# Optimization experiments

Hardware: AMD Instinct MI355X
Metric: run time of the kernel (lower is better)

Reference implementation:

```python
import jax, jax.numpy as jnp
import numpy as np

NP = 4            # num_patches
P = NP * NP       # num_patches^2
BIG = 1e8         # self-distance sentinel used by the torch module
IN_CH = 128
MID = IN_CH // 2
NUM_CONVS = 3
KS = 3
B, H, W = 4, 256, 256


def conv2d(x, w, b):
    # x: [B,C,H,W], w: [O,I,kh,kw] (OIHW), stride 1, 'same' padding
    pad = (w.shape[-1] - 1) // 2
    y = jax.lax.conv_general_dilated(
        x, w, window_strides=(1, 1), padding=[(pad, pad), (pad, pad)],
        dimension_numbers=('NCHW', 'OIHW', 'NCHW'))
    return y + b[None, :, None, None]


def patchify(x):
    # [B,C,H,W] -> [B,P,C,hs,ws] with row-major patch order (i*NP+j)
    b, c, h, w = x.shape
    hs, ws = h // NP, w // NP
    x = x.reshape(b, c, NP, hs, NP, ws).transpose(0, 2, 4, 1, 3, 5)
    return x.reshape(b, P, c, hs, ws)


def unpatchify(xp, h, w):
    b, p, c, hs, ws = xp.shape
    x = xp.reshape(b, NP, NP, c, hs, ws).transpose(0, 3, 1, 4, 2, 5)
    return x.reshape(b, c, h, w)


def setup_inputs() -> dict:
    key = jax.random.key(0)
    ks = jax.random.split(key, 16)
    s = 0.05  # weight init scale (~kaiming for these fan-ins)
    inp = {
        'x':     jax.random.normal(ks[0], (B, IN_CH, H, W), jnp.float32),
        'pre_w': jax.random.normal(ks[1], (MID, IN_CH, KS, KS), jnp.float32) * s,
        'pre_b': jnp.zeros((MID,), jnp.float32),
        'c1_w':  jax.random.normal(ks[2], (NUM_CONVS, MID, MID, KS, KS), jnp.float32) * s,
        'c1_b':  jnp.zeros((NUM_CONVS, MID), jnp.float32),
        'c2_w':  jax.random.normal(ks[3], (NUM_CONVS, MID, MID, KS, KS), jnp.float32) * s,
        'c2_b':  jnp.zeros((NUM_CONVS, MID), jnp.float32),
        'p1_w':  jax.random.normal(ks[4], (P, MID, MID), jnp.float32) * s,  # [patch, out, in] 1x1 conv
        'p1_b':  jnp.zeros((P, MID), jnp.float32),
        'p2_w':  jax.random.normal(ks[5], (P, MID, MID), jnp.float32) * s,
        'p2_b':  jnp.zeros((P, MID), jnp.float32),
        'fin_w': jax.random.normal(ks[6], (IN_CH, IN_CH, KS, KS), jnp.float32) * s,
        'fin_b': jnp.zeros((IN_CH,), jnp.float32),
    }
    return inp


def reference(x, pre_w, pre_b, c1_w, c1_b, c2_w, c2_b,
              p1_w, p1_b, p2_w, p2_b, fin_w, fin_b):
    x0 = jax.nn.relu(conv2d(x, pre_w, pre_b))
    h1 = x0
    for i in range(c1_w.shape[0]):
        h1 = jax.nn.relu(conv2d(h1, c1_w[i], c1_b[i]))
    x1 = h1 + x0
    h2 = x0
    for i in range(c2_w.shape[0]):
        h2 = jax.nn.relu(conv2d(h2, c2_w[i], c2_b[i]))
    x2 = h2 + x0

    # per-patch 1x1 convs (all P patches batched via einsum)
    x1p = patchify(x1)  # [B,P,C,hs,ws]
    x2p = patchify(x2)
    x1p = jnp.einsum('bpchw,pdc->bpdhw', x1p, p1_w) + p1_b[None, :, :, None, None]
    x2p = jnp.einsum('bpchw,pdc->bpdhw', x2p, p2_w) + p2_b[None, :, :, None, None]

    # pairwise squared distances between x1 patches and x2 patches
    f1 = x1p.reshape(B, P, -1)
    f2 = x2p.reshape(B, P, -1)
    d = ((f1 ** 2).sum(-1)[:, :, None]
         + (f2 ** 2).sum(-1)[:, None, :]
         - 2.0 * jnp.einsum('bpd,bqd->bpq', f1, f2))  # [B,P,P]
    d = jnp.where(jnp.eye(P, dtype=bool)[None], BIG, d)
    # torch does softmax(exp(-d)) — keep the double transform faithfully
    attn = jax.nn.softmax(jnp.exp(-d), axis=-1)  # [B,P,P]

    outp = jnp.einsum('bpq,bqchw->bpchw', attn, x2p)
    out = unpatchify(outp, H, W)           # [B,MID,H,W]
    out = jnp.concatenate([out, x0], axis=1)  # [B,IN_CH,H,W]
    out = jax.nn.relu(conv2d(out, fin_w, fin_b))
    return out + x
```

## Files before the change

### kernel.cpp

```cpp
#include <hip/hip_runtime.h>
#include <hip/hip_bf16.h>

#define BB   4
#define HH   256
#define WW   256
#define INCH 128
#define MIDC 64
#define NPAT 4
#define PP   16
#define PS   64

typedef __bf16 bf16x8 __attribute__((ext_vector_type(8)));
typedef float f32x4 __attribute__((ext_vector_type(4)));
typedef unsigned short ushort_t;

#define UPL 16777216UL

__device__ inline ushort_t f2bf(float f) {
    unsigned u = __float_as_uint(f);
    unsigned r = (u + 0x7FFFu + ((u >> 16) & 1u)) >> 16;
    return (ushort_t)r;
}
__device__ inline float bf2f(ushort_t h) {
    return __uint_as_float(((unsigned)h) << 16);
}
__device__ inline f32x4 mfma16(uint4 a, uint4 b, f32x4 c) {
    return __builtin_amdgcn_mfma_f32_16x16x32_bf16(
        __builtin_bit_cast(bf16x8, a), __builtin_bit_cast(bf16x8, b), c, 0, 0, 0);
}

__global__ __launch_bounds__(256) void prep_all_kernel(
    const float* __restrict__ pre_w, const float* __restrict__ c1_w,
    const float* __restrict__ c2_w,  const float* __restrict__ fin_w,
    const float* __restrict__ p1_w,  const float* __restrict__ p2_w,
    const float* __restrict__ c1_b,  const float* __restrict__ c2_b,
    ushort_t* __restrict__ wpPre, ushort_t* __restrict__ wpC,
    ushort_t* __restrict__ wpFin, ushort_t* __restrict__ pw1b,
    ushort_t* __restrict__ pw2b,  float* __restrict__ zbuf,
    float* __restrict__ cbias)
{
    int idx = blockIdx.x * 256 + threadIdx.x;
    if (idx < 73728) {
        int tap = idx % 9, ci = (idx / 9) % 128, co = idx / 1152;
        wpPre[(tap * 64 + co) * 128 + ci] = f2bf(pre_w[idx]);
    } else if (idx < 294912) {
        int j = idx - 73728;
        int which = j / 36864, k = j % 36864;
        const float* src = (which < 3) ? (c1_w + (size_t)which * 36864)
                                       : (c2_w + (size_t)(which - 3) * 36864);
        int tap = k % 9, ci = (k / 9) % 64, co = k / 576;
        wpC[(size_t)which * 36864 + (tap * 64 + co) * 64 + ci] = f2bf(src[k]);
    } else if (idx < 442368) {
        int k = idx - 294912;
        int tap = k % 9, ci = (k / 9) % 128, co = k / 1152;
        wpFin[(tap * 128 + co) * 128 + ci] = f2bf(fin_w[k]);
    } else if (idx < 507904) {
        pw1b[idx - 442368] = f2bf(p1_w[idx - 442368]);
    } else if (idx < 573440) {
        pw2b[idx - 507904] = f2bf(p2_w[idx - 507904]);
    } else if (idx < 574592) {
        zbuf[idx - 573440] = 0.f;
    } else if (idx < 574784) {
        cbias[idx - 574592] = c1_b[idx - 574592];
    } else if (idx < 574976) {
        cbias[192 + idx - 574784] = c2_b[idx - 574784];
    }
}

__global__ __launch_bounds__(256) void x_to_nhwc_kernel(
    const float* __restrict__ x, ushort_t* __restrict__ xh)
{
    __shared__ ushort_t sm[64 * 136];
    const int t = threadIdx.x;
    const int bx = blockIdx.x;
    const int b = bx >> 10;
    const int pxbase = (bx & 1023) * 64;
#pragma unroll
    for (int i = 0; i < 32; ++i) {
        int idx = i * 256 + t;
        int c = idx >> 6, pxl = idx & 63;
        sm[pxl * 136 + c] = f2bf(x[((size_t)(b * 128 + c)) * 65536 + pxbase + pxl]);
    }
    __syncthreads();
#pragma unroll
    for (int i = 0; i < 4; ++i) {
        int idx = i * 256 + t;
        int pxl = idx >> 4, q = idx & 15;
        uint4 v = *(const uint4*)&sm[pxl * 136 + q * 8];
        *(uint4*)(xh + ((size_t)b * 65536 + pxbase + pxl) * 128 + q * 8) = v;
    }
}

template<int CIN, int CSPLIT>
__device__ inline void stage10x34(const ushort_t* inA, const ushort_t* inB,
                                  int b, int y0, int x0, int t, int cb,
                                  uint4 (&stg)[6])
{
#pragma unroll
    for (int i = 0; i < 6; ++i) {
        int e = i * 256 + t;
        int pxl = e >> 2, quad = e & 3;
        int row = pxl / 34, xl = pxl - row * 34;
        int gy = y0 + row - 1, gx = x0 + xl - 1;
        bool ok = (e < 1360) && ((unsigned)gy < 256u) && ((unsigned)gx < 256u);
        int c0 = cb + quad * 8;
        const ushort_t* src; int nch, ch;
        if ((CSPLIT == CIN) || (c0 < CSPLIT)) { src = inA; nch = CSPLIT; ch = c0; }
        else { src = inB; nch = CIN - CSPLIT; ch = c0 - CSPLIT; }
        uint4 v = make_uint4(0u, 0u, 0u, 0u);
        if (ok) v = *(const uint4*)(src + ((size_t)((b * 256 + gy) * 256 + gx)) * nch + ch);
        stg[i] = v;
    }
}

template<int CIN, int CSPLIT, int OMODE, bool PAIR, bool COPAIR>
__global__ __launch_bounds__(256) void mconv3x3(
    const ushort_t* __restrict__ inA, const ushort_t* __restrict__ inB,
    const ushort_t* __restrict__ wgtT,
    const float* __restrict__ bias,
    const void* __restrict__ res,
    void* __restrict__ out,
    int COUT, size_t inStride, size_t wStride, size_t bStride, size_t outStride)
{
    constexpr int NCH = CIN / 32;
    __shared__ ushort_t sm[10 * 34 * 36];

    const int t = threadIdx.x;
    const int nx = gridDim.x;
    const int bid = blockIdx.x;
    const int fid = (bid & 7) * (nx >> 3) + (bid >> 3);
    int tile, cog;
    if (COPAIR) { tile = fid >> 1; cog = (fid & 1) * 64; }
    else        { tile = fid;      cog = PAIR ? 0 : blockIdx.y * 64; }
    const int y0 = (tile >> 3) * 8;
    const int x0 = (tile & 7) * 32;
    const int br = PAIR ? blockIdx.y : 0;
    const ushort_t* inAb = inA + (size_t)br * inStride;
    const ushort_t* inBb = inB + (size_t)br * inStride;
    const ushort_t* wgt  = wgtT + (size_t)br * wStride;
    const float*    bs   = bias + (size_t)br * bStride;
    const int b = blockIdx.z;
    const int l = t & 63, w = t >> 6;
    const int lan15 = l & 15;
    const int g4 = l >> 4;
    const int k8 = g4 * 8;
    const int co0 = cog + (w & 1) * 32;
    const int xw = (w >> 1) * 16;

    f32x4 acc[2][8];
#pragma unroll
    for (int mt = 0; mt < 2; ++mt)
#pragma unroll
        for (int r = 0; r < 8; ++r) acc[mt][r] = (f32x4)0.f;

    uint4 stg[6];
    stage10x34<CIN, CSPLIT>(inAb, inBb, b, y0, x0, t, 0, stg);

    for (int cc = 0; cc < NCH; ++cc) {
        __syncthreads();
#pragma unroll
        for (int i = 0; i < 6; ++i) {
            int e = i * 256 + t;
            if (e < 1360) {
                int pxl = e >> 2, quad = e & 3;
                *(uint4*)&sm[pxl * 36 + quad * 8] = stg[i];
            }
        }
        __syncthreads();
        if (cc + 1 < NCH)
            stage10x34<CIN, CSPLIT>(inAb, inBb, b, y0, x0, t, (cc + 1) * 32, stg);

        const int cb = cc * 32;
        uint4 af[2][9];
#pragma unroll
        for (int mt = 0; mt < 2; ++mt)
#pragma unroll
            for (int tap = 0; tap < 9; ++tap)
                af[mt][tap] = *(const uint4*)(wgt +
                    ((size_t)tap * COUT + co0 + mt * 16 + lan15) * CIN + cb + k8);

#pragma unroll
        for (int s = 0; s < 10; ++s) {
#pragma unroll
            for (int dx = 0; dx < 3; ++dx) {
                const int pxl = s * 34 + xw + lan15 + dx;
                uint4 bv = *(const uint4*)&sm[pxl * 36 + k8];
#pragma unroll
                for (int dy = 0; dy < 3; ++dy) {
                    const int r = s - dy;
                    if (r >= 0 && r < 8) {
                        acc[0][r] = mfma16(af[0][dy * 3 + dx], bv, acc[0][r]);
                        acc[1][r] = mfma16(af[1][dy * 3 + dx], bv, acc[1][r]);
                    }
                }
            }
        }
    }

#pragma unroll
    for (int mt = 0; mt < 2; ++mt) {
#pragma unroll
        for (int r = 0; r < 8; ++r) {
            const int y = y0 + r;
            const int x = x0 + xw + lan15;
            const int codr = co0 + mt * 16 + g4 * 4;
            float v[4];
#pragma unroll
            for (int j = 0; j < 4; ++j)
                v[j] = fmaxf(acc[mt][r][j] + bs[codr + j], 0.f);
            if constexpr (OMODE == 2) {
                const float* rf = (const float*)res;
                float* of = (float*)out;
#pragma unroll
                for (int j = 0; j < 4; ++j) {
                    size_t oi = ((size_t)(b * COUT + codr + j) * 256 + y) * 256 + x;
                    of[oi] = v[j] + rf[oi];
                }
            } else {
                const size_t pix = (size_t)(b * 256 + y) * 256 + x;
                if constexpr (OMODE == 1) {
                    const ushort_t* rp = (const ushort_t*)res + pix * 64 + codr;
#pragma unroll
                    for (int j = 0; j < 4; ++j) v[j] += bf2f(rp[j]);
                }
                uint2 pk;
                pk.x = (unsigned)f2bf(v[0]) | ((unsigned)f2bf(v[1]) << 16);
                pk.y = (unsigned)f2bf(v[2]) | ((unsigned)f2bf(v[3]) << 16);
                *(uint2*)((ushort_t*)out + (size_t)br * outStride + pix * COUT + codr) = pk;
            }
        }
    }
}

__global__ __launch_bounds__(256) void patch1x1_mfma(
    const ushort_t* __restrict__ in0, const ushort_t* __restrict__ pwb0,
    const float* __restrict__ bias1, const float* __restrict__ bias2,
    ushort_t* __restrict__ outp0, float* __restrict__ nrm0)
{
    __shared__ ushort_t smp[256 * 72];
    const int side = blockIdx.z;
    const ushort_t* in  = in0  + (size_t)side * UPL;
    const ushort_t* pwb = pwb0 + side * 65536;
    const float*   bias = side ? bias2 : bias1;
    ushort_t*      outp = outp0 + (size_t)side * UPL;
    float*         nrm  = nrm0 + side * 64;

    const int t = threadIdx.x;
    const int bx = blockIdx.x;
    const int bp = blockIdx.y;
    const int b = bp >> 4, p = bp & 15;
    const int py = (p >> 2) * 64, px0 = (p & 3) * 64;
    const int l = t & 63, w = t >> 6;
    const int lan15 = l & 15, k8 = (l >> 4) * 8;

#pragma unroll
    for (int i = 0; i < 8; ++i) {
        int idx = i * 256 + t;
        int px = idx >> 3, q = idx & 7;
        int y = py + bx * 4 + (px >> 6), x = px0 + (px & 63);
        uint4 v = *(const uint4*)(in + ((size_t)(b * 256 + y) * 256 + x) * 64 + q * 8);
        *(uint4*)&smp[px * 72 + q * 8] = v;
    }
    __syncthreads();

    uint4 af[4][2];
#pragma unroll
    for (int mt = 0; mt < 4; ++mt)
#pragma unroll
        for (int kk = 0; kk < 2; ++kk)
            af[mt][kk] = *(const uint4*)(pwb + (size_t)p * 4096 +
                                         (mt * 16 + lan15) * 64 + kk * 32 + k8);

    f32x4 acc[4][4];
#pragma unroll
    for (int mt = 0; mt < 4; ++mt)
#pragma unroll
        for (int j = 0; j < 4; ++j) acc[mt][j] = (f32x4)0.f;

#pragma unroll
    for (int kk = 0; kk < 2; ++kk)
#pragma unroll
        for (int j = 0; j < 4; ++j) {
            int px = (w * 4 + j) * 16 + lan15;
            uint4 bv = *(const uint4*)&smp[px * 72 + kk * 32 + k8];
#pragma unroll
            for (int mt = 0; mt < 4; ++mt)
                acc[mt][j] = mfma16(af[mt][kk], bv, acc[mt][j]);
        }

    float nsum = 0.f;
#pragma unroll
    for (int mt = 0; mt < 4; ++mt)
#pragma unroll
        for (int j = 0; j < 4; ++j) {
            int px = (w * 4 + j) * 16 + lan15;
            int y = py + bx * 4 + (px >> 6), x = px0 + (px & 63);
            int d0 = mt * 16 + (l >> 4) * 4;
            float v[4];
#pragma unroll
            for (int r = 0; r < 4; ++r) {
                v[r] = acc[mt][j][r] + bias[p * 64 + d0 + r];
                nsum = fmaf(v[r], v[r], nsum);
            }
            uint2 pk;
            pk.x = (unsigned)f2bf(v[0]) | ((unsigned)f2bf(v[1]) << 16);
            pk.y = (unsigned)f2bf(v[2]) | ((unsigned)f2bf(v[3]) << 16);
            *(uint2*)(outp + ((size_t)(b * 256 + y) * 256 + x) * 64 + d0) = pk;
        }

#pragma unroll
    for (int off = 32; off > 0; off >>= 1) nsum += __shfl_down(nsum, off);
    if (l == 0) atomicAdd(&nrm[b * 16 + p], nsum);
}

__global__ __launch_bounds__(256) void patch_dots_mfma(
    const ushort_t* __restrict__ f1, const ushort_t* __restrict__ f2,
    float* __restrict__ dotv)
{
    __shared__ float rbuf[4][64][4];
    const int t = threadIdx.x;
    const int kb = blockIdx.x;
    const int b = blockIdx.y;
    const int l = t & 63, w = t >> 6;
    const int lan15 = l & 15, k8q = (l >> 4) * 8;
    const int p = lan15;
    const int py = (p >> 2) * 64, px0 = (p & 3) * 64;
    const size_t rowbase = ((size_t)(b * 256 + py + kb) * 256 + px0) * 64;

    f32x4 acc = (f32x4)0.f;
    for (int ixl = 0; ixl < 16; ++ixl) {
        const size_t pa = rowbase + (size_t)(w * 16 + ixl) * 64 + k8q;
#pragma unroll
        for (int c0 = 0; c0 < 64; c0 += 32) {
            uint4 av = *(const uint4*)(f1 + pa + c0);
            uint4 bv = *(const uint4*)(f2 + pa + c0);
            acc = mfma16(av, bv, acc);
        }
    }
#pragma unroll
    for (int r = 0; r < 4; ++r) rbuf[w][l][r] = acc[r];
    __syncthreads();
    if (t < 64) {
#pragma unroll
        for (int r = 0; r < 4; ++r) {
            float s = rbuf[0][t][r] + rbuf[1][t][r] + rbuf[2][t][r] + rbuf[3][t][r];
            int pp = (t >> 4) * 4 + r, qq = t & 15;
            atomicAdd(&dotv[b * 256 + pp * 16 + qq], s);
        }
    }
}

__global__ __launch_bounds__(1024) void attn_kernel(
    const float* __restrict__ n1, const float* __restrict__ n2,
    const float* __restrict__ dotv, float* __restrict__ attn)
{
    __shared__ float tv[1024];
    int t = threadIdx.x;
    int b = t >> 8, p = (t >> 4) & 15, q = t & 15;
    float d = n1[b * 16 + p] + n2[b * 16 + q] - 2.f * dotv[t];
    if (p == q) d = 1e8f;
    float e = expf(-d);
    tv[t] = e;
    __syncthreads();
    const float* row = &tv[(t >> 4) << 4];
    float m = row[0];
#pragma unroll
    for (int j = 1; j < 16; ++j) m = fmaxf(m, row[j]);
    float ssum = 0.f;
#pragma unroll
    for (int j = 0; j < 16; ++j) ssum += expf(row[j] - m);
    attn[t] = expf(e - m) / ssum;
}

__global__ __launch_bounds__(256) void combine_kernel(
    const float* __restrict__ attn, const ushort_t* __restrict__ x2p,
    ushort_t* __restrict__ cmb)
{
    int gid = blockIdx.x * 256 + threadIdx.x;
    int cq = gid & 7;
    int pxg = (gid >> 3) & 65535;
    int b = gid >> 19;
    int y = pxg >> 8, x = pxg & 255;
    int p = (y >> 6) * 4 + (x >> 6);
    int i = y & 63, j = x & 63;
    const float* arow = attn + (size_t)(b * 16 + p) * 16;
    float s[8];
#pragma unroll
    for (int k = 0; k < 8; ++k) s[k] = 0.f;
#pragma unroll
    for (int q = 0; q < 16; ++q) {
        float a = arow[q];
        const ushort_t* sp = x2p +
            ((size_t)(b * 256 + (q >> 2) * 64 + i) * 256 + (q & 3) * 64 + j) * 64 + cq * 8;
        uint4 v = *(const uint4*)sp;
        unsigned uu[4] = {v.x, v.y, v.z, v.w};
#pragma unroll
        for (int h = 0; h < 4; ++h) {
            s[h * 2]     = fmaf(a, bf2f((ushort_t)(uu[h] & 0xffffu)), s[h * 2]);
            s[h * 2 + 1] = fmaf(a, bf2f((ushort_t)(uu[h] >> 16)),     s[h * 2 + 1]);
        }
    }
    uint4 o;
    o.x = (unsigned)f2bf(s[0]) | ((unsigned)f2bf(s[1]) << 16);
    o.y = (unsigned)f2bf(s[2]) | ((unsigned)f2bf(s[3]) << 16);
    o.z = (unsigned)f2bf(s[4]) | ((unsigned)f2bf(s[5]) << 16);
    o.w = (unsigned)f2bf(s[6]) | ((unsigned)f2bf(s[7]) << 16);
    *(uint4*)(cmb + ((size_t)b * 65536 + pxg) * 64 + cq * 8) = o;
}

extern "C" void kernel_launch(void* const* d_in, const int* in_sizes, int n_in,
                              void* d_out, int out_size, void* d_ws, size_t ws_size,
                              hipStream_t stream)
{
    const float* x     = (const float*)d_in[0];
    const float* pre_w = (const float*)d_in[1];
    const float* pre_b = (const float*)d_in[2];
    const float* c1_w  = (const float*)d_in[3];
    const float* c1_b  = (const float*)d_in[4];
    const float* c2_w  = (const float*)d_in[5];
    const float* c2_b  = (const float*)d_in[6];
    const float* p1_w  = (const float*)d_in[7];
    const float* p1_b  = (const float*)d_in[8];
    const float* p2_w  = (const float*)d_in[9];
    const float* p2_b  = (const float*)d_in[10];
    const float* fin_w = (const float*)d_in[11];
    const float* fin_b = (const float*)d_in[12];

    float* out = (float*)d_out;
    ushort_t* wsu = (ushort_t*)d_ws;

    const size_t U = UPL;

    ushort_t* xh   = wsu;
    ushort_t* x0b  = wsu + 2 * U;
    ushort_t* tA   = wsu;
    ushort_t* tB   = wsu + 3 * U;
    ushort_t* x12b = (ushort_t*)d_out;
    ushort_t* x1p  = tB;
    ushort_t* x2p  = tB + U;
    ushort_t* cmb  = wsu;

    ushort_t* wpPre = wsu + 5 * U;
    ushort_t* wpC   = wpPre + 73728;
    ushort_t* wpFin = wpC + 6 * 36864;
    ushort_t* pw1b  = wpFin + 147456;
    ushort_t* pw2b  = pw1b + 65536;
    float* n1    = (float*)(pw2b + 65536);
    float* n2    = n1 + 64;
    float* dotv  = n2 + 64;
    float* attn  = dotv + 1024;
    float* cbias = attn + 1024;

    const dim3 blk(256);

    prep_all_kernel<<<(574976 + 255) / 256, blk, 0, stream>>>(
        pre_w, c1_w, c2_w, fin_w, p1_w, p2_w, c1_b, c2_b,
        wpPre, wpC, wpFin, pw1b, pw2b, n1, cbias);

    x_to_nhwc_kernel<<<4096, blk, 0, stream>>>(x, xh);

    const dim3 g64(256, 1, BB);
    const dim3 gPair(256, 2, BB);
    const dim3 gFin(512, 1, BB);

    mconv3x3<128, 128, 0, false, false><<<g64, blk, 0, stream>>>(
        xh, xh, wpPre, pre_b, nullptr, x0b, 64, 0, 0, 0, 0);

    mconv3x3<64, 64, 0, true, false><<<gPair, blk, 0, stream>>>(
        x0b, x0b, wpC, cbias, nullptr, tA, 64,
        0, 3 * 36864, 192, U);
    mconv3x3<64, 64, 0, true, false><<<gPair, blk, 0, stream>>>(
        tA, tA, wpC + 36864, cbias + 64, nullptr, tB, 64,
        U, 3 * 36864, 192, U);
    mconv3x3<64, 64, 1, true, false><<<gPair, blk, 0, stream>>>(
        tB, tB, wpC + 2 * 36864, cbias + 128, x0b, x12b, 64,
        U, 3 * 36864, 192, U);

    const dim3 pgrid(16, BB * PP, 2);
    patch1x1_mfma<<<pgrid, blk, 0, stream>>>(x12b, pw1b, p1_b, p2_b, x1p, n1);

    const dim3 dgrid(64, BB);
    patch_dots_mfma<<<dgrid, blk, 0, stream>>>(x1p, x2p, dotv);

    attn_kernel<<<1, 1024, 0, stream>>>(n1, n2, dotv, attn);

    combine_kernel<<<BB * 65536 * 8 / 256, blk, 0, stream>>>(attn, x2p, cmb);

    mconv3x3<128, 64, 2, false, true><<<gFin, blk, 0, stream>>>(
        cmb, x0b, wpFin, fin_b, x, out, 128, 0, 0, 0, 0);
}
```

Before: 579.4 us.

## Use 4x64 wide tiles for the pre-conv and final conv

Adds a wconv3x3 kernel that tiles the output as 4 rows by 64 columns, with each wave covering 2 rows. Each loaded LDS input row is reused across two output rows (drow), so shared-memory reads per MFMA drop and the halo overhead changes shape. The 128-input-channel convs (pre and final) switch to this kernel, and the 64-channel branch convs stay on the old kernel. The new tile also drops LDS padding (32-channel stride instead of 36), which may raise bank conflicts.

```diff
diff --git a/kernel.cpp b/kernel.cpp
--- a/kernel.cpp
+++ b/kernel.cpp
@@ -113,7 +113,29 @@
     }
 }
 
-template<int CIN, int CSPLIT, int OMODE, bool PAIR, bool COPAIR>
+template<int CIN, int CSPLIT>
+__device__ inline void stage6x68(const ushort_t* inA, const ushort_t* inB,
+                                 int b, int y0, int x0, int t, int cb,
+                                 uint4 (&stg)[7])
+{
+#pragma unroll
+    for (int i = 0; i < 7; ++i) {
+        int e = i * 256 + t;
+        int pxl = e >> 2, quad = e & 3;
+        int row = pxl / 68, xl = pxl - row * 68;
+        int gy = y0 + row - 1, gx = x0 + xl - 1;
+        bool ok = (e < 1632) && ((unsigned)gy < 256u) && ((unsigned)gx < 256u);
+        int c0 = cb + quad * 8;
+        const ushort_t* src; int nch, ch;
+        if ((CSPLIT == CIN) || (c0 < CSPLIT)) { src = inA; nch = CSPLIT; ch = c0; }
+        else { src = inB; nch = CIN - CSPLIT; ch = c0 - CSPLIT; }
+        uint4 v = make_uint4(0u, 0u, 0u, 0u);
+        if (ok) v = *(const uint4*)(src + ((size_t)((b * 256 + gy) * 256 + gx)) * nch + ch);
+        stg[i] = v;
+    }
+}
+
+template<int CIN, int CSPLIT, int OMODE, bool PAIR>
 __global__ __launch_bounds__(256) void mconv3x3(
     const ushort_t* __restrict__ inA, const ushort_t* __restrict__ inB,
     const ushort_t* __restrict__ wgtT,
@@ -129,9 +151,8 @@
     const int nx = gridDim.x;
     const int bid = blockIdx.x;
     const int fid = (bid & 7) * (nx >> 3) + (bid >> 3);
-    int tile, cog;
-    if (COPAIR) { tile = fid >> 1; cog = (fid & 1) * 64; }
-    else        { tile = fid;      cog = PAIR ? 0 : blockIdx.y * 64; }
+    const int tile = fid;
+    const int cog = PAIR ? 0 : blockIdx.y * 64;
     const int y0 = (tile >> 3) * 8;
     const int x0 = (tile & 7) * 32;
     const int br = PAIR ? blockIdx.y : 0;
@@ -208,6 +229,116 @@
 #pragma unroll
             for (int j = 0; j < 4; ++j)
                 v[j] = fmaxf(acc[mt][r][j] + bs[codr + j], 0.f);
+            const size_t pix = (size_t)(b * 256 + y) * 256 + x;
+            if constexpr (OMODE == 1) {
+                const ushort_t* rp = (const ushort_t*)res + pix * 64 + codr;
+#pragma unroll
+                for (int j = 0; j < 4; ++j) v[j] += bf2f(rp[j]);
+            }
+            uint2 pk;
+            pk.x = (unsigned)f2bf(v[0]) | ((unsigned)f2bf(v[1]) << 16);
+            pk.y = (unsigned)f2bf(v[2]) | ((unsigned)f2bf(v[3]) << 16);
+            *(uint2*)((ushort_t*)out + (size_t)br * outStride + pix * COUT + codr) = pk;
+        }
+    }
+}
+
+template<int CIN, int CSPLIT, int OMODE, bool COPAIR>
+__global__ __launch_bounds__(256) void wconv3x3(
+    const ushort_t* __restrict__ inA, const ushort_t* __restrict__ inB,
+    const ushort_t* __restrict__ wgtT,
+    const float* __restrict__ bias,
+    const void* __restrict__ res,
+    void* __restrict__ out,
+    int COUT)
+{
+    constexpr int NCH = CIN / 32;
+    __shared__ ushort_t sm[6 * 68 * 32];
+
+    const int t = threadIdx.x;
+    const int nx = gridDim.x;
+    const int bid = blockIdx.x;
+    const int fid = (bid & 7) * (nx >> 3) + (bid >> 3);
+    int tile, cog;
+    if (COPAIR) { tile = fid >> 1; cog = (fid & 1) * 64; }
+    else        { tile = fid;      cog = blockIdx.y * 64; }
+    const int y0 = (tile >> 2) * 4;
+    const int x0 = (tile & 3) * 64;
+    const int b = blockIdx.z;
+    const int l = t & 63, w = t >> 6;
+    const int lan15 = l & 15;
+    const int g4 = l >> 4;
+    const int k8 = g4 * 8;
+    const int co0 = cog + (w & 1) * 32;
+    const int wrow0 = (w >> 1) * 2;
+
+    f32x4 acc[2][8];
+#pragma unroll
+    for (int mt = 0; mt < 2; ++mt)
+#pragma unroll
+        for (int nt = 0; nt < 8; ++nt) acc[mt][nt] = (f32x4)0.f;
+
+    uint4 stg[7];
+    stage6x68<CIN, CSPLIT>(inA, inB, b, y0, x0, t, 0, stg);
+
+    for (int cc = 0; cc < NCH; ++cc) {
+        __syncthreads();
+#pragma unroll
+        for (int i = 0; i < 7; ++i) {
+            int e = i * 256 + t;
+            if (e < 1632) {
+                int pxl = e >> 2, quad = e & 3;
+                *(uint4*)&sm[pxl * 32 + quad * 8] = stg[i];
+            }
+        }
+        __syncthreads();
+        if (cc + 1 < NCH)
+            stage6x68<CIN, CSPLIT>(inA, inB, b, y0, x0, t, (cc + 1) * 32, stg);
+
+        const int cb = cc * 32;
+        uint4 af[2][9];
+#pragma unroll
+        for (int mt = 0; mt < 2; ++mt)
+#pragma unroll
+            for (int tap = 0; tap < 9; ++tap)
+                af[mt][tap] = *(const uint4*)(wgtT +
+                    ((size_t)tap * COUT + co0 + mt * 16 + lan15) * CIN + cb + k8);
+
+#pragma unroll
+        for (int rr = 0; rr < 4; ++rr) {
+            const int r = wrow0 + rr;
+#pragma unroll
+            for (int col = 0; col < 4; ++col) {
+#pragma unroll
+                for (int dx = 0; dx < 3; ++dx) {
+                    const int xc = col * 16 + lan15 + dx;
+                    uint4 bv = *(const uint4*)&sm[(r * 68 + xc) * 32 + k8];
+#pragma unroll
+                    for (int drow = 0; drow < 2; ++drow) {
+                        const int dy = rr - drow;
+                        if (dy >= 0 && dy < 3) {
+                            const int tap = dy * 3 + dx;
+                            const int nt = drow * 4 + col;
+                            acc[0][nt] = mfma16(af[0][tap], bv, acc[0][nt]);
+                            acc[1][nt] = mfma16(af[1][tap], bv, acc[1][nt]);
+                        }
+                    }
+                }
+            }
+        }
+    }
+
+#pragma unroll
+    for (int mt = 0; mt < 2; ++mt) {
+#pragma unroll
+        for (int nt = 0; nt < 8; ++nt) {
+            const int y = y0 + wrow0 + (nt >> 2);
+            const int x = x0 + (nt & 3) * 16 + lan15;
+            const int codr = co0 + mt * 16 + g4 * 4;
+            float v[4];
+#pragma unroll
+            for (int j = 0; j < 4; ++j)
+                v[j] = fmaxf(acc[mt][nt][j] + bias[codr + j], 0.f);
             if constexpr (OMODE == 2) {
                 const float* rf = (const float*)res;
                 float* of = (float*)out;
@@ -218,15 +349,10 @@
                 }
             } else {
                 const size_t pix = (size_t)(b * 256 + y) * 256 + x;
-                if constexpr (OMODE == 1) {
-                    const ushort_t* rp = (const ushort_t*)res + pix * 64 + codr;
-#pragma unroll
-                    for (int j = 0; j < 4; ++j) v[j] += bf2f(rp[j]);
-                }
                 uint2 pk;
                 pk.x = (unsigned)f2bf(v[0]) | ((unsigned)f2bf(v[1]) << 16);
                 pk.y = (unsigned)f2bf(v[2]) | ((unsigned)f2bf(v[3]) << 16);
-                *(uint2*)((ushort_t*)out + (size_t)br * outStride + pix * COUT + codr) = pk;
+                *(uint2*)((ushort_t*)out + pix * COUT + codr) = pk;
             }
         }
     }
@@ -459,20 +585,20 @@
 
     x_to_nhwc_kernel<<<4096, blk, 0, stream>>>(x, xh);
 
-    const dim3 g64(256, 1, BB);
+    const dim3 gWide(256, 1, BB);
     const dim3 gPair(256, 2, BB);
     const dim3 gFin(512, 1, BB);
 
-    mconv3x3<128, 128, 0, false, false><<<g64, blk, 0, stream>>>(
-        xh, xh, wpPre, pre_b, nullptr, x0b, 64, 0, 0, 0, 0);
-
-    mconv3x3<64, 64, 0, true, false><<<gPair, blk, 0, stream>>>(
+    wconv3x3<128, 128, 0, false><<<gWide, blk, 0, stream>>>(
+        xh, xh, wpPre, pre_b, nullptr, x0b, 64);
+
+    mconv3x3<64, 64, 0, true><<<gPair, blk, 0, stream>>>(
         x0b, x0b, wpC, cbias, nullptr, tA, 64,
         0, 3 * 36864, 192, U);
-    mconv3x3<64, 64, 0, true, false><<<gPair, blk, 0, stream>>>(
+    mconv3x3<64, 64, 0, true><<<gPair, blk, 0, stream>>>(
         tA, tA, wpC + 36864, cbias + 64, nullptr, tB, 64,
         U, 3 * 36864, 192, U);
-    mconv3x3<64, 64, 1, true, false><<<gPair, blk, 0, stream>>>(
+    mconv3x3<64, 64, 1, true><<<gPair, blk, 0, stream>>>(
         tB, tB, wpC + 2 * 36864, cbias + 128, x0b, x12b, 64,
         U, 3 * 36864, 192, U);
 
@@ -486,6 +612,6 @@
 
     combine_kernel<<<BB * 65536 * 8 / 256, blk, 0, stream>>>(attn, x2p, cmb);
 
-    mconv3x3<128, 64, 2, false, true><<<gFin, blk, 0, stream>>>(
-        cmb, x0b, wpFin, fin_b, x, out, 128, 0, 0, 0, 0);
-}
+    wconv3x3<128, 64, 2, true><<<gFin, blk, 0, stream>>>(
+        cmb, x0b, wpFin, fin_b, x, out, 128);
+}
```

Result: faster. 540.2 us (-6.8%).

## Reshape 3x3 conv tiles from 8x32 to 4x64 pixels per block

Applied to the files above, without the earlier changes.

Changes the conv kernel's spatial tile from 8 rows by 32 columns to 4 rows by 64 columns. Each wave now covers two output rows across four 16-pixel column groups and loops over input rows to reuse shared-memory fragments across vertical taps. This adds halo (6x68 vs 10x34) and more shared-memory fragment reads per MFMA. It also removes the LDS row padding (stride 36 to 32), which may introduce bank conflicts.

```diff
diff --git a/kernel.cpp b/kernel.cpp
--- a/kernel.cpp
+++ b/kernel.cpp
@@ -92,17 +92,17 @@
 }
 
 template<int CIN, int CSPLIT>
-__device__ inline void stage10x34(const ushort_t* inA, const ushort_t* inB,
-                                  int b, int y0, int x0, int t, int cb,
-                                  uint4 (&stg)[6])
-{
-#pragma unroll
-    for (int i = 0; i < 6; ++i) {
+__device__ inline void stage6x68(const ushort_t* inA, const ushort_t* inB,
+                                 int b, int y0, int x0, int t, int cb,
+                                 uint4 (&stg)[7])
+{
+#pragma unroll
+    for (int i = 0; i < 7; ++i) {
         int e = i * 256 + t;
         int pxl = e >> 2, quad = e & 3;
-        int row = pxl / 34, xl = pxl - row * 34;
+        int row = pxl / 68, xl = pxl - row * 68;
         int gy = y0 + row - 1, gx = x0 + xl - 1;
-        bool ok = (e < 1360) && ((unsigned)gy < 256u) && ((unsigned)gx < 256u);
+        bool ok = (e < 1632) && ((unsigned)gy < 256u) && ((unsigned)gx < 256u);
         int c0 = cb + quad * 8;
         const ushort_t* src; int nch, ch;
         if ((CSPLIT == CIN) || (c0 < CSPLIT)) { src = inA; nch = CSPLIT; ch = c0; }
@@ -114,7 +114,7 @@
 }
 
 template<int CIN, int CSPLIT, int OMODE, bool PAIR, bool COPAIR>
-__global__ __launch_bounds__(256) void mconv3x3(
+__global__ __launch_bounds__(256) void wconv3x3(
     const ushort_t* __restrict__ inA, const ushort_t* __restrict__ inB,
     const ushort_t* __restrict__ wgtT,
     const float* __restrict__ bias,
@@ -123,7 +123,7 @@
     int COUT, size_t inStride, size_t wStride, size_t bStride, size_t outStride)
 {
     constexpr int NCH = CIN / 32;
-    __shared__ ushort_t sm[10 * 34 * 36];
+    __shared__ ushort_t sm[6 * 68 * 32];
 
     const int t = threadIdx.x;
     const int nx = gridDim.x;
@@ -132,8 +132,8 @@
     int tile, cog;
     if (COPAIR) { tile = fid >> 1; cog = (fid & 1) * 64; }
     else        { tile = fid;      cog = PAIR ? 0 : blockIdx.y * 64; }
-    const int y0 = (tile >> 3) * 8;
-    const int x0 = (tile & 7) * 32;
+    const int y0 = (tile >> 2) * 4;
+    const int x0 = (tile & 3) * 64;
     const int br = PAIR ? blockIdx.y : 0;
     const ushort_t* inAb = inA + (size_t)br * inStride;
     const ushort_t* inBb = inB + (size_t)br * inStride;
@@ -145,30 +145,30 @@
     const int g4 = l >> 4;
     const int k8 = g4 * 8;
     const int co0 = cog + (w & 1) * 32;
-    const int xw = (w >> 1) * 16;
+    const int wrow0 = (w >> 1) * 2;
 
     f32x4 acc[2][8];
 #pragma unroll
     for (int mt = 0; mt < 2; ++mt)
 #pragma unroll
-        for (int r = 0; r < 8; ++r) acc[mt][r] = (f32x4)0.f;
-
-    uint4 stg[6];
-    stage10x34<CIN, CSPLIT>(inAb, inBb, b, y0, x0, t, 0, stg);
+        for (int nt = 0; nt < 8; ++nt) acc[mt][nt] = (f32x4)0.f;
+
+    uint4 stg[7];
+    stage6x68<CIN, CSPLIT>(inAb, inBb, b, y0, x0, t, 0, stg);
 
     for (int cc = 0; cc < NCH; ++cc) {
         __syncthreads();
 #pragma unroll
-        for (int i = 0; i < 6; ++i) {
+        for (int i = 0; i < 7; ++i) {
             int e = i * 256 + t;
-            if (e < 1360) {
+            if (e < 1632) {
                 int pxl = e >> 2, quad = e & 3;
-                *(uint4*)&sm[pxl * 36 + quad * 8] = stg[i];
+                *(uint4*)&sm[pxl * 32 + quad * 8] = stg[i];
             }
         }
         __syncthreads();
         if (cc + 1 < NCH)
-            stage10x34<CIN, CSPLIT>(inAb, inBb, b, y0, x0, t, (cc + 1) * 32, stg);
+            stage6x68<CIN, CSPLIT>(inAb, inBb, b, y0, x0, t, (cc + 1) * 32, stg);
 
         const int cb = cc * 32;
         uint4 af[2][9];
@@ -180,17 +180,23 @@
                     ((size_t)tap * COUT + co0 + mt * 16 + lan15) * CIN + cb + k8);
 
 #pragma unroll
-        for (int s = 0; s < 10; ++s) {
-#pragma unroll
-            for (int dx = 0; dx < 3; ++dx) {
-                const int pxl = s * 34 + xw + lan15 + dx;
-                uint4 bv = *(const uint4*)&sm[pxl * 36 + k8];
-#pragma unroll
-                for (int dy = 0; dy < 3; ++dy) {
-                    const int r = s - dy;
-                    if (r >= 0 && r < 8) {
-                        acc[0][r] = mfma16(af[0][dy * 3 + dx], bv, acc[0][r]);
-                        acc[1][r] = mfma16(af[1][dy * 3 + dx], bv, acc[1][r]);
+        for (int rr = 0; rr < 4; ++rr) {
+            const int r = wrow0 + rr;
+#pragma unroll
+            for (int col = 0; col < 4; ++col) {
+#pragma unroll
+                for (int dx = 0; dx < 3; ++dx) {
+                    const int xc = col * 16 + lan15 + dx;
+                    uint4 bv = *(const uint4*)&sm[(r * 68 + xc) * 32 + k8];
+#pragma unroll
+                    for (int drow = 0; drow < 2; ++drow) {
+                        const int dy = rr - drow;
+                        if (dy >= 0 && dy < 3) {
+                            const int tap = dy * 3 + dx;
+                            const int nt = drow * 4 + col;
+                            acc[0][nt] = mfma16(af[0][tap], bv, acc[0][nt]);
+                            acc[1][nt] = mfma16(af[1][tap], bv, acc[1][nt]);
+                        }
                     }
                 }
             }
@@ -200,14 +206,14 @@
 #pragma unroll
     for (int mt = 0; mt < 2; ++mt) {
 #pragma unroll
-        for (int r = 0; r < 8; ++r) {
-            const int y = y0 + r;
-            const int x = x0 + xw + lan15;
+        for (int nt = 0; nt < 8; ++nt) {
+            const int y = y0 + wrow0 + (nt >> 2);
+            const int x = x0 + (nt & 3) * 16 + lan15;
             const int codr = co0 + mt * 16 + g4 * 4;
             float v[4];
 #pragma unroll
             for (int j = 0; j < 4; ++j)
-                v[j] = fmaxf(acc[mt][r][j] + bs[codr + j], 0.f);
+                v[j] = fmaxf(acc[mt][nt][j] + bias[(size_t)br * bStride + codr + j], 0.f);
             if constexpr (OMODE == 2) {
                 const float* rf = (const float*)res;
                 float* of = (float*)out;
@@ -459,20 +465,20 @@
 
     x_to_nhwc_kernel<<<4096, blk, 0, stream>>>(x, xh);
 
-    const dim3 g64(256, 1, BB);
+    const dim3 gWide(256, 1, BB);
     const dim3 gPair(256, 2, BB);
     const dim3 gFin(512, 1, BB);
 
-    mconv3x3<128, 128, 0, false, false><<<g64, blk, 0, stream>>>(
+    wconv3x3<128, 128, 0, false, false><<<gWide, blk, 0, stream>>>(
         xh, xh, wpPre, pre_b, nullptr, x0b, 64, 0, 0, 0, 0);
 
-    mconv3x3<64, 64, 0, true, false><<<gPair, blk, 0, stream>>>(
+    wconv3x3<64, 64, 0, true, false><<<gPair, blk, 0, stream>>>(
         x0b, x0b, wpC, cbias, nullptr, tA, 64,
         0, 3 * 36864, 192, U);
-    mconv3x3<64, 64, 0, true, false><<<gPair, blk, 0, stream>>>(
+    wconv3x3<64, 64, 0, true, false><<<gPair, blk, 0, stream>>>(
         tA, tA, wpC + 36864, cbias + 64, nullptr, tB, 64,
         U, 3 * 36864, 192, U);
-    mconv3x3<64, 64, 1, true, false><<<gPair, blk, 0, stream>>>(
+    wconv3x3<64, 64, 1, true, false><<<gPair, blk, 0, stream>>>(
         tB, tB, wpC + 2 * 36864, cbias + 128, x0b, x12b, 64,
         U, 3 * 36864, 192, U);
 
@@ -486,6 +492,6 @@
 
     combine_kernel<<<BB * 65536 * 8 / 256, blk, 0, stream>>>(attn, x2p, cmb);
 
-    mconv3x3<128, 64, 2, false, true><<<gFin, blk, 0, stream>>>(
+    wconv3x3<128, 64, 2, false, true><<<gFin, blk, 0, stream>>>(
         cmb, x0b, wpFin, fin_b, x, out, 128, 0, 0, 0, 0);
 }
```

New measurement: 606.6 us. 4.7% more time.
